# Optimization experiments

Hardware: AMD Instinct MI355X
Metric: run time of the kernel (lower is better)

## Reference

```python
import jax, jax.numpy as jnp
import numpy as np

B, L, H, A = 2, 384, 256, 14  # batch, total residues (binder+target), hidden, atoms/residue


def setup_inputs() -> dict:
    key = jax.random.key(0)
    ks = jax.random.split(key, 8)
    s = 1.0 / np.sqrt(H)
    h = jax.random.normal(ks[0], (B, L, H), jnp.float32)          # encoder output
    X = jax.random.normal(ks[1], (B, L, A, 3), jnp.float32)       # coordinates
    mask = jnp.ones((B, L), jnp.int32)                             # residue validity mask
    Wx_w = jax.random.normal(ks[2], (H, H), jnp.float32) * s
    Wx_b = jnp.zeros((H,), jnp.float32)
    Ux_w = jax.random.normal(ks[3], (H, H), jnp.float32) * s
    Ux_b = jnp.zeros((H,), jnp.float32)
    Tx_w = jax.random.normal(ks[4], (A, H), jnp.float32) * s
    Tx_b = jnp.zeros((A,), jnp.float32)
    return dict(h=h, X=X, mask=mask, Wx_w=Wx_w, Wx_b=Wx_b,
                Ux_w=Ux_w, Ux_b=Ux_b, Tx_w=Tx_w, Tx_b=Tx_b)


def reference(h, X, mask, Wx_w, Wx_b, Ux_w, Ux_b, Tx_w, Tx_b):
    # One recurrent coordinate-update step of FADocker._forward.
    m = mask.astype(h.dtype)                                   # (B, L)
    hw = h @ Wx_w.T + Wx_b                                     # (B, L, H)  = W_x(h)
    hu = h @ Ux_w.T + Ux_b                                     # (B, L, H)  = U_x(h)
    mij = hw[:, :, None, :] + hu[:, None, :, :]                # (B, L, L, H)
    gate = jnp.einsum('bijh,ah->bija', jax.nn.relu(mij), Tx_w) + Tx_b  # (B, L, L, A) = T_x(mij)
    xij = (X[:, :, None] - X[:, None, :]) * gate[..., None]   # (B, L, L, A, 3)
    f = jnp.einsum('bijac,bj->biac', xij, m)                   # masked sum over j
    f = f / (1e-6 + m.sum(axis=1)[:, None, None, None])        # (B, L, A, 3)
    return X + jnp.clip(f, -20.0, 20.0)
```

## Files before the change

kernel.cpp:

```cpp
#include <hip/hip_runtime.h>
#include <hip/hip_bf16.h>

#define HDIM 256
#define LDIM 384
#define BDIM 2
#define ADIM 14

typedef __attribute__((ext_vector_type(8))) short bf16x8;
typedef __attribute__((ext_vector_type(4))) float f32x4;

static __device__ __forceinline__ unsigned pack_bf16(float x, float y) {
    __hip_bfloat162 t = __float22bfloat162_rn(make_float2(x, y));
    return *reinterpret_cast<unsigned*>(&t);
}

__global__ __launch_bounds__(256) void k_gemm(
    const float* __restrict__ h,
    const float* __restrict__ Wx_w, const float* __restrict__ Wx_b,
    const float* __restrict__ Ux_w, const float* __restrict__ Ux_b,
    float* __restrict__ hw, unsigned* __restrict__ huP)
{
    __shared__ float hsT[32][34];
    __shared__ float wsT[32][34];
    const int t  = threadIdx.x;
    const int tx = t & 15, ty = t >> 4;
    const int row0 = blockIdx.y * 32;
    const int col0 = blockIdx.x * 32;

    const int lr = t & 31;
    const int lk = (t >> 5) * 4;
    const float* __restrict__ hrow = &h[(row0 + lr) * HDIM];
    const int c_l = col0 + lr;
    const float* __restrict__ wrow = (c_l < HDIM) ? &Wx_w[c_l * HDIM]
                                                  : &Ux_w[(c_l - HDIM) * HDIM];

    float a00 = 0.f, a01 = 0.f, a10 = 0.f, a11 = 0.f;

    for (int k0 = 0; k0 < HDIM; k0 += 32) {
        const float4 hv = *(const float4*)&hrow[k0 + lk];
        const float4 wv = *(const float4*)&wrow[k0 + lk];
        hsT[lk + 0][lr] = hv.x; hsT[lk + 1][lr] = hv.y;
        hsT[lk + 2][lr] = hv.z; hsT[lk + 3][lr] = hv.w;
        wsT[lk + 0][lr] = wv.x; wsT[lk + 1][lr] = wv.y;
        wsT[lk + 2][lr] = wv.z; wsT[lk + 3][lr] = wv.w;
        __syncthreads();
        #pragma unroll
        for (int kk = 0; kk < 32; ++kk) {
            const float2 av = *(const float2*)&hsT[kk][ty * 2];
            const float2 bv = *(const float2*)&wsT[kk][tx * 2];
            a00 = fmaf(av.x, bv.x, a00); a01 = fmaf(av.x, bv.y, a01);
            a10 = fmaf(av.y, bv.x, a10); a11 = fmaf(av.y, bv.y, a11);
        }
        __syncthreads();
    }

    const int row = row0 + ty * 2;
    const int b = row / LDIM, i0 = row % LDIM;
    const int c0 = col0 + tx * 2;
    if (c0 < HDIM) {
        const float b0 = Wx_b[c0], b1 = Wx_b[c0 + 1];
        *(float2*)&hw[row * HDIM + c0]       = make_float2(a00 + b0, a01 + b1);
        *(float2*)&hw[(row + 1) * HDIM + c0] = make_float2(a10 + b0, a11 + b1);
    } else {
        const int ch = c0 - HDIM;
        const float b0 = Ux_b[ch], b1 = Ux_b[ch + 1];
        uint2 pv;
        pv.x = pack_bf16(a00 + b0, a01 + b1);
        pv.y = pack_bf16(a10 + b0, a11 + b1);
        *(uint2*)&huP[(b * (HDIM / 2) + (ch >> 1)) * LDIM + i0] = pv;
    }
}

__global__ __launch_bounds__(384) void k_main(
    const float* __restrict__ hw, const unsigned* __restrict__ huP,
    const float* __restrict__ X, const int* __restrict__ mask,
    const float* __restrict__ Tx_w, const float* __restrict__ Tx_b,
    float* __restrict__ out)
{
    __shared__ unsigned TxP[16 * 130];
    __shared__ float m_lds[LDIM];
    __shared__ float part2[24 * 16 * 4];
    __shared__ float part_m[24];

    const int i = blockIdx.x, b = blockIdx.y;
    const int tid = threadIdx.x;
    const int w = tid >> 6;
    const int lane = tid & 63;
    const int n = lane & 15;
    const int quad = lane >> 4;

    for (int idx = tid; idx < 16 * 128; idx += 384) {
        const int nn = idx >> 7, k2 = idx & 127;
        unsigned v = 0;
        if (nn < ADIM) {
            const float2 tw = *(const float2*)&Tx_w[nn * HDIM + 2 * k2];
            v = pack_bf16(tw.x, tw.y);
        }
        TxP[nn * 130 + k2] = v;
    }
    m_lds[tid] = (float)mask[b * LDIM + tid];
    __syncthreads();

    const float* __restrict__ hwrow = &hw[(b * LDIM + i) * HDIM];
    const unsigned* __restrict__ hub = &huP[b * (HDIM / 2) * LDIM];

    f32x4 acc[4];
    #pragma unroll
    for (int t = 0; t < 4; ++t) acc[t] = (f32x4){0.f, 0.f, 0.f, 0.f};

    const int jbase = w * 64 + n;

    #pragma unroll 2
    for (int kc = 0; kc < 8; ++kc) {
        union { unsigned u[4]; bf16x8 v; } bu;
        const int bofs = n * 130 + kc * 16 + quad * 4;
        *(uint2*)&bu.u[0] = *(const uint2*)&TxP[bofs];
        *(uint2*)&bu.u[2] = *(const uint2*)&TxP[bofs + 2];
        const float4 hwa = *(const float4*)(hwrow + kc * 32 + quad * 8);
        const float4 hwb = *(const float4*)(hwrow + kc * 32 + quad * 8 + 4);
        const float hv[8] = {hwa.x, hwa.y, hwa.z, hwa.w, hwb.x, hwb.y, hwb.z, hwb.w};
        const int h2base = kc * 16 + quad * 4;
        #pragma unroll
        for (int t = 0; t < 4; ++t) {
            const unsigned* __restrict__ hp = &hub[h2base * LDIM + jbase + t * 16];
            union { unsigned u[4]; bf16x8 v; } au;
            #pragma unroll
            for (int d = 0; d < 4; ++d) {
                const unsigned pk = hp[d * LDIM];
                const float lo = __uint_as_float(pk << 16);
                const float hi = __uint_as_float(pk & 0xffff0000u);
                const float t0 = fmaxf(hv[2 * d] + lo, 0.f);
                const float t1 = fmaxf(hv[2 * d + 1] + hi, 0.f);
                au.u[d] = pack_bf16(t0, t1);
            }
            acc[t] = __builtin_amdgcn_mfma_f32_16x16x32_bf16(au.v, bu.v, acc[t], 0, 0, 0);
        }
    }

    float s1 = 0.f, s2x = 0.f, s2y = 0.f, s2z = 0.f, pm = 0.f;
    if (n < ADIM) {
        const float txb = Tx_b[n];
        #pragma unroll
        for (int t = 0; t < 4; ++t) {
            #pragma unroll
            for (int r = 0; r < 4; ++r) {
                const int jd = (w * 4 + t) * 16 + quad * 4 + r;
                const float m = m_lds[jd];
                const float g = acc[t][r] + txb;
                const float mg = m * g;
                const float* __restrict__ Xp = &X[((b * LDIM + jd) * ADIM + n) * 3];
                s1 += mg;
                s2x = fmaf(mg, Xp[0], s2x);
                s2y = fmaf(mg, Xp[1], s2y);
                s2z = fmaf(mg, Xp[2], s2z);
                pm += m;
            }
        }
    }
    {
        f32x4 sv = {s2x, s2y, s2z, s1};
        *(f32x4*)&part2[((w * 4 + quad) * 16 + n) * 4] = sv;
    }
    if (n == 0) part_m[w * 4 + quad] = pm;
    __syncthreads();

    if (tid < 42) {
        const int a = tid / 3, c = tid % 3;
        float S2 = 0.f, S1 = 0.f, msum = 0.f;
        #pragma unroll 4
        for (int g = 0; g < 24; ++g) {
            const float* __restrict__ p = &part2[(g * 16 + a) * 4];
            S2 += p[c]; S1 += p[3]; msum += part_m[g];
        }
        const float denom = 1e-6f + msum;
        const int idx = ((b * LDIM + i) * ADIM + a) * 3 + c;
        const float xi = X[idx];
        float f = (xi * S1 - S2) / denom;
        f = fminf(fmaxf(f, -20.f), 20.f);
        out[idx] = xi + f;
    }
}

extern "C" void kernel_launch(void* const* d_in, const int* in_sizes, int n_in,
                              void* d_out, int out_size, void* d_ws, size_t ws_size,
                              hipStream_t stream) {
    (void)in_sizes; (void)n_in; (void)out_size; (void)ws_size;
    const float* h    = (const float*)d_in[0];
    const float* X    = (const float*)d_in[1];
    const int*   mask = (const int*)  d_in[2];
    const float* Wx_w = (const float*)d_in[3];
    const float* Wx_b = (const float*)d_in[4];
    const float* Ux_w = (const float*)d_in[5];
    const float* Ux_b = (const float*)d_in[6];
    const float* Tx_w = (const float*)d_in[7];
    const float* Tx_b = (const float*)d_in[8];
    float* out = (float*)d_out;

    float*    hw  = (float*)d_ws;
    unsigned* huP = (unsigned*)(hw + BDIM * LDIM * HDIM);

    k_gemm<<<dim3(16, 24), dim3(256), 0, stream>>>(h, Wx_w, Wx_b, Ux_w, Ux_b, hw, huP);
    k_main<<<dim3(LDIM, BDIM), 384, 0, stream>>>(hw, huP, X, mask, Tx_w, Tx_b, out);
}
```

Baseline: 99.18 us.

## Rewrite projection GEMM with bf16 MFMA, one wavefront per 32x32 tile

Replaces the fp32 LDS-tiled SIMT GEMM that computes W_x(h) and U_x(h) with a single-wavefront kernel. It loads fp32 rows directly from global memory, converts them to bf16, and issues 16x16x32 bf16 MFMA instructions on four accumulators per 32x32 tile. This removes the shared-memory staging and barriers and moves the FLOPs onto matrix cores. In exchange, hw is now computed from bf16-rounded inputs, which lowers precision, and 64-thread blocks mean far fewer threads per block.

```diff
diff --git a/kernel.cpp b/kernel.cpp
--- a/kernel.cpp
+++ b/kernel.cpp
@@ -5,6 +5,7 @@
 #define LDIM 384
 #define BDIM 2
 #define ADIM 14
+#define H2 (HDIM / 2)
 
 typedef __attribute__((ext_vector_type(8))) short bf16x8;
 typedef __attribute__((ext_vector_type(4))) float f32x4;
@@ -14,60 +15,79 @@
     return *reinterpret_cast<unsigned*>(&t);
 }
 
-__global__ __launch_bounds__(256) void k_gemm(
+static __device__ __forceinline__ bf16x8 cvt8(float4 a, float4 b) {
+    union { unsigned u[4]; bf16x8 v; } r;
+    r.u[0] = pack_bf16(a.x, a.y); r.u[1] = pack_bf16(a.z, a.w);
+    r.u[2] = pack_bf16(b.x, b.y); r.u[3] = pack_bf16(b.z, b.w);
+    return r.v;
+}
+
+__global__ __launch_bounds__(64) void k_gemm(
     const float* __restrict__ h,
     const float* __restrict__ Wx_w, const float* __restrict__ Wx_b,
     const float* __restrict__ Ux_w, const float* __restrict__ Ux_b,
     float* __restrict__ hw, unsigned* __restrict__ huP)
 {
-    __shared__ float hsT[32][34];
-    __shared__ float wsT[32][34];
-    const int t  = threadIdx.x;
-    const int tx = t & 15, ty = t >> 4;
+    const int lane = threadIdx.x;
+    const int n = lane & 15;
+    const int quad = lane >> 4;
+
+    const int c0   = blockIdx.x * 32;
     const int row0 = blockIdx.y * 32;
-    const int col0 = blockIdx.x * 32;
-
-    const int lr = t & 31;
-    const int lk = (t >> 5) * 4;
-    const float* __restrict__ hrow = &h[(row0 + lr) * HDIM];
-    const int c_l = col0 + lr;
-    const float* __restrict__ wrow = (c_l < HDIM) ? &Wx_w[c_l * HDIM]
-                                                  : &Ux_w[(c_l - HDIM) * HDIM];
-
-    float a00 = 0.f, a01 = 0.f, a10 = 0.f, a11 = 0.f;
-
-    for (int k0 = 0; k0 < HDIM; k0 += 32) {
-        const float4 hv = *(const float4*)&hrow[k0 + lk];
-        const float4 wv = *(const float4*)&wrow[k0 + lk];
-        hsT[lk + 0][lr] = hv.x; hsT[lk + 1][lr] = hv.y;
-        hsT[lk + 2][lr] = hv.z; hsT[lk + 3][lr] = hv.w;
-        wsT[lk + 0][lr] = wv.x; wsT[lk + 1][lr] = wv.y;
-        wsT[lk + 2][lr] = wv.z; wsT[lk + 3][lr] = wv.w;
-        __syncthreads();
-        #pragma unroll
-        for (int kk = 0; kk < 32; ++kk) {
-            const float2 av = *(const float2*)&hsT[kk][ty * 2];
-            const float2 bv = *(const float2*)&wsT[kk][tx * 2];
-            a00 = fmaf(av.x, bv.x, a00); a01 = fmaf(av.x, bv.y, a01);
-            a10 = fmaf(av.y, bv.x, a10); a11 = fmaf(av.y, bv.y, a11);
-        }
-        __syncthreads();
-    }
-
-    const int row = row0 + ty * 2;
-    const int b = row / LDIM, i0 = row % LDIM;
-    const int c0 = col0 + tx * 2;
+
+    const float* __restrict__ wbase = (c0 < HDIM) ? &Wx_w[c0 * HDIM]
+                                                  : &Ux_w[(c0 - HDIM) * HDIM];
+    const float* __restrict__ wl0 = wbase + (n) * HDIM + quad * 8;
+    const float* __restrict__ wl1 = wbase + (16 + n) * HDIM + quad * 8;
+    const float* __restrict__ hl0 = h + (row0 + n) * HDIM + quad * 8;
+    const float* __restrict__ hl1 = h + (row0 + 16 + n) * HDIM + quad * 8;
+
+    f32x4 acc00 = {0,0,0,0}, acc01 = {0,0,0,0}, acc10 = {0,0,0,0}, acc11 = {0,0,0,0};
+
+    #pragma unroll 4
+    for (int kc = 0; kc < 8; ++kc) {
+        const int ko = kc * 32;
+        const bf16x8 a0 = cvt8(*(const float4*)(wl0 + ko), *(const float4*)(wl0 + ko + 4));
+        const bf16x8 a1 = cvt8(*(const float4*)(wl1 + ko), *(const float4*)(wl1 + ko + 4));
+        const bf16x8 b0 = cvt8(*(const float4*)(hl0 + ko), *(const float4*)(hl0 + ko + 4));
+        const bf16x8 b1 = cvt8(*(const float4*)(hl1 + ko), *(const float4*)(hl1 + ko + 4));
+        acc00 = __builtin_amdgcn_mfma_f32_16x16x32_bf16(a0, b0, acc00, 0, 0, 0);
+        acc01 = __builtin_amdgcn_mfma_f32_16x16x32_bf16(a0, b1, acc01, 0, 0, 0);
+        acc10 = __builtin_amdgcn_mfma_f32_16x16x32_bf16(a1, b0, acc10, 0, 0, 0);
+        acc11 = __builtin_amdgcn_mfma_f32_16x16x32_bf16(a1, b1, acc11, 0, 0, 0);
+    }
+
+    const int grow0 = row0 + n;
+    const int grow1 = row0 + 16 + n;
+    const int b = row0 / LDIM;
+    const int i0 = grow0 - b * LDIM, i1 = grow1 - b * LDIM;
+
     if (c0 < HDIM) {
-        const float b0 = Wx_b[c0], b1 = Wx_b[c0 + 1];
-        *(float2*)&hw[row * HDIM + c0]       = make_float2(a00 + b0, a01 + b1);
-        *(float2*)&hw[(row + 1) * HDIM + c0] = make_float2(a10 + b0, a11 + b1);
+        #pragma unroll
+        for (int ct = 0; ct < 2; ++ct) {
+            const int cb = c0 + ct * 16 + quad * 4;
+            const float4 bias = *(const float4*)&Wx_b[cb];
+            const f32x4 aR0 = ct ? acc10 : acc00;
+            const f32x4 aR1 = ct ? acc11 : acc01;
+            *(float4*)&hw[grow0 * HDIM + cb] =
+                make_float4(aR0[0] + bias.x, aR0[1] + bias.y, aR0[2] + bias.z, aR0[3] + bias.w);
+            *(float4*)&hw[grow1 * HDIM + cb] =
+                make_float4(aR1[0] + bias.x, aR1[1] + bias.y, aR1[2] + bias.z, aR1[3] + bias.w);
+        }
     } else {
-        const int ch = c0 - HDIM;
-        const float b0 = Ux_b[ch], b1 = Ux_b[ch + 1];
-        uint2 pv;
-        pv.x = pack_bf16(a00 + b0, a01 + b1);
-        pv.y = pack_bf16(a10 + b0, a11 + b1);
-        *(uint2*)&huP[(b * (HDIM / 2) + (ch >> 1)) * LDIM + i0] = pv;
+        unsigned* __restrict__ hub = &huP[b * H2 * LDIM];
+        #pragma unroll
+        for (int ct = 0; ct < 2; ++ct) {
+            const int ch = (c0 - HDIM) + ct * 16 + quad * 4;
+            const float4 bias = *(const float4*)&Ux_b[ch];
+            const f32x4 aR0 = ct ? acc10 : acc00;
+            const f32x4 aR1 = ct ? acc11 : acc01;
+            const int h2 = ch >> 1;
+            hub[(h2)     * LDIM + i0] = pack_bf16(aR0[0] + bias.x, aR0[1] + bias.y);
+            hub[(h2 + 1) * LDIM + i0] = pack_bf16(aR0[2] + bias.z, aR0[3] + bias.w);
+            hub[(h2)     * LDIM + i1] = pack_bf16(aR1[0] + bias.x, aR1[1] + bias.y);
+            hub[(h2 + 1) * LDIM + i1] = pack_bf16(aR1[2] + bias.z, aR1[3] + bias.w);
+        }
     }
 }
 
@@ -102,7 +122,7 @@
     __syncthreads();
 
     const float* __restrict__ hwrow = &hw[(b * LDIM + i) * HDIM];
-    const unsigned* __restrict__ hub = &huP[b * (HDIM / 2) * LDIM];
+    const unsigned* __restrict__ hub = &huP[b * H2 * LDIM];
 
     f32x4 acc[4];
     #pragma unroll
@@ -199,6 +219,6 @@
     float*    hw  = (float*)d_ws;
     unsigned* huP = (unsigned*)(hw + BDIM * LDIM * HDIM);
 
-    k_gemm<<<dim3(16, 24), dim3(256), 0, stream>>>(h, Wx_w, Wx_b, Ux_w, Ux_b, hw, huP);
+    k_gemm<<<dim3(16, 24), dim3(64), 0, stream>>>(h, Wx_w, Wx_b, Ux_w, Ux_b, hw, huP);
     k_main<<<dim3(LDIM, BDIM), 384, 0, stream>>>(hw, huP, X, mask, Tx_w, Tx_b, out);
 }
```

Measured after the change: 92.47 us. 6.8% less time.
